# Performance work log

Measured on AMD Instinct MI355X. Metric: run time of the kernel, lower is better.

The kernel has to match this reference:

```python
import jax, jax.numpy as jnp
import numpy as np


def setup_inputs() -> dict:
    key = jax.random.key(0)
    k1, k2, k3, k4 = jax.random.split(key, 4)
    N, E, F_IN, F_OUT = 50000, 800000, 128, 128
    x = jax.random.normal(k1, (N, F_IN), dtype=jnp.float32)
    src = jax.random.randint(k2, (E,), 0, N, dtype=jnp.int32)
    dst = jax.random.randint(k3, (E,), 0, N, dtype=jnp.int32)
    # Linear(2*in, out, bias=False) weight, torch layout (out, 2*in)
    W = jax.random.normal(k4, (F_OUT, 2 * F_IN), dtype=jnp.float32) * (1.0 / np.sqrt(2 * F_IN))
    return {"x": x, "src": src, "dst": dst, "num_nodes": N, "W": W}


def reference(x, src, dst, num_nodes, W):
    # Mean aggregation over sparse adjacency (edge list src -> dst):
    # aggregated[v] = mean_{u in N(v)} x[u]
    msgs = x[src]                                            # [E, F] gather
    summed = jax.ops.segment_sum(msgs, dst, num_segments=num_nodes)  # [N, F]
    deg = jax.ops.segment_sum(jnp.ones_like(dst, dtype=x.dtype), dst,
                              num_segments=num_nodes)        # [N]
    agg = summed / jnp.maximum(deg, 1.0)[:, None]            # mean, safe for isolated nodes
    h = jnp.concatenate([x, agg], axis=1)                    # [N, 2F]
    out = h @ W.T                                            # [N, F_out]
    return jax.nn.relu(out)
```

## Files before the change

### kernel.cpp

```cpp
#include <hip/hip_runtime.h>
#include <hip/hip_bf16.h>

typedef __attribute__((ext_vector_type(8))) short short8;
typedef __attribute__((ext_vector_type(4))) float f32x4;
typedef __attribute__((ext_vector_type(2))) float f32x2;

#define BKS      6
#define BKN      64
#define ITERA    16
#define NBMAX    1024
#define CAPB_MAX 3072

__device__ __forceinline__ unsigned short f2bf(float f) {
    unsigned u = __builtin_bit_cast(unsigned, f);
    u += 0x7fffu + ((u >> 16) & 1u);
    return (unsigned short)(u >> 16);
}
__device__ __forceinline__ float bf2f(unsigned short b) {
    return __builtin_bit_cast(float, ((unsigned)b) << 16);
}

__global__ __launch_bounds__(256) void prepbin_kernel(
    const float* __restrict__ x, unsigned short* __restrict__ xb,
    unsigned char* __restrict__ xq,
    const float* __restrict__ W, unsigned short* __restrict__ Wp,
    const int* __restrict__ src, const int* __restrict__ dst,
    unsigned* gcur, unsigned* __restrict__ gbuf,
    int E, int nb, int capb, int nx8)
{
    __shared__ unsigned cnt[NBMAX];
    __shared__ unsigned gbase[NBMAX];
    int tid = threadIdx.x;
    int gid = blockIdx.x * 256 + tid;
    int gstr = gridDim.x * 256;

    for (int i = gid; i < nx8; i += gstr) {
        const float4* p = (const float4*)(x + (size_t)i * 8);
        float4 lo = p[0], hi = p[1];
        short8 v;
        v[0] = (short)f2bf(lo.x); v[1] = (short)f2bf(lo.y);
        v[2] = (short)f2bf(lo.z); v[3] = (short)f2bf(lo.w);
        v[4] = (short)f2bf(hi.x); v[5] = (short)f2bf(hi.y);
        v[6] = (short)f2bf(hi.z); v[7] = (short)f2bf(hi.w);
        *(short8*)(xb + (size_t)i * 8) = v;

        int p0 = 0, p1 = 0;
        p0 = __builtin_amdgcn_cvt_pk_fp8_f32(lo.x, lo.y, p0, false);
        p0 = __builtin_amdgcn_cvt_pk_fp8_f32(lo.z, lo.w, p0, true);
        p1 = __builtin_amdgcn_cvt_pk_fp8_f32(hi.x, hi.y, p1, false);
        p1 = __builtin_amdgcn_cvt_pk_fp8_f32(hi.z, hi.w, p1, true);
        uint2 q; q.x = (unsigned)p0; q.y = (unsigned)p1;
        *(uint2*)(xq + (size_t)i * 8) = q;
    }
    if (gid < 4096) {
        const float4* p = (const float4*)(W + (size_t)gid * 8);
        float4 lo = p[0], hi = p[1];
        short8 v;
        v[0] = (short)f2bf(lo.x); v[1] = (short)f2bf(lo.y);
        v[2] = (short)f2bf(lo.z); v[3] = (short)f2bf(lo.w);
        v[4] = (short)f2bf(hi.x); v[5] = (short)f2bf(hi.y);
        v[6] = (short)f2bf(hi.z); v[7] = (short)f2bf(hi.w);
        int r    = gid >> 5;
        int c0   = (gid & 31) << 3;
        int ct   = r >> 4;
        int arow = r & 15;
        int ks   = c0 >> 5;
        int kgrp = (c0 >> 3) & 3;
        int l    = arow | (kgrp << 4);
        *(short8*)(Wp + (((size_t)(ct * 8 + ks) * 64 + l) * 8)) = v;
    }

    int EB = (E + 256 * ITERA - 1) / (256 * ITERA);
    if (blockIdx.x < EB) {
        for (int t = tid; t < nb; t += 256) cnt[t] = 0u;
        __syncthreads();

        int e0 = blockIdx.x * (256 * ITERA) + tid;
        unsigned pk[ITERA];
        unsigned short bk[ITERA], pp[ITERA];
#pragma unroll
        for (int it = 0; it < ITERA; ++it) {
            int e = e0 + it * 256;
            bk[it] = 0xFFFFu;
            if (e < E) {
                int d = dst[e];
                unsigned b = (unsigned)d >> BKS;
                pk[it] = (unsigned)src[e] | ((unsigned)(d & (BKN - 1)) << 24);
                pp[it] = (unsigned short)atomicAdd(&cnt[b], 1u);
                bk[it] = (unsigned short)b;
            }
        }
        __syncthreads();
        for (int t = tid; t < nb; t += 256)
            gbase[t] = cnt[t] ? atomicAdd(&gcur[t], cnt[t]) : 0u;
        __syncthreads();
#pragma unroll
        for (int it = 0; it < ITERA; ++it) {
            if (bk[it] != 0xFFFFu) {
                unsigned b = bk[it];
                unsigned off = gbase[b] + pp[it];
                if (off < (unsigned)capb) gbuf[(size_t)b * capb + off] = pk[it];
            }
        }
    }
}

__global__ __launch_bounds__(512) void agg_gemm_kernel(
    const unsigned short* __restrict__ xb,
    const unsigned char* __restrict__ xq,
    const unsigned* __restrict__ gbuf,
    const unsigned* __restrict__ gcur,
    const unsigned short* __restrict__ Wp,
    float* __restrict__ out, int N, int capb)
{
    __shared__ unsigned cnt[BKN];
    __shared__ unsigned degs[BKN];
    __shared__ unsigned cur[BKN];
    __shared__ unsigned elist[CAPB_MAX];
    __shared__ unsigned short aggs[BKN][136];

    int tid = threadIdx.x;
    int b   = blockIdx.x;
    unsigned cntB = gcur[b];
    if (cntB > (unsigned)capb) cntB = (unsigned)capb;
    const unsigned* bb = gbuf + (size_t)b * capb;

    if (tid < BKN) cnt[tid] = 0u;
    __syncthreads();
    for (unsigned i = tid; i < cntB; i += 512)
        atomicAdd(&cnt[bb[i] >> 24], 1u);
    __syncthreads();
    if (tid < BKN) degs[tid] = cnt[tid];
    __syncthreads();
#pragma unroll
    for (int off = 1; off < BKN; off <<= 1) {
        unsigned t = (tid < BKN && tid >= off) ? cnt[tid - off] : 0u;
        __syncthreads();
        if (tid < BKN) cnt[tid] += t;
        __syncthreads();
    }
    if (tid < BKN) cur[tid] = cnt[tid] - degs[tid];
    __syncthreads();
    for (unsigned i = tid; i < cntB; i += 512) {
        unsigned pk = bb[i];
        unsigned p  = atomicAdd(&cur[pk >> 24], 1u);
        elist[p] = pk & 0x00FFFFFFu;
    }
    __syncthreads();

    int wv = tid >> 6, l = tid & 63;
    int q4 = l >> 4, ql = l & 15;
    int base = b << BKS;

#pragma unroll
    for (int pass = 0; pass < BKN / 32; ++pass) {
        int r0 = pass * 32 + wv * 4 + q4;
        unsigned endi  = cnt[r0];
        unsigned dg    = degs[r0];
        unsigned start = endi - dg;
        float acc[8] = {0.f, 0.f, 0.f, 0.f, 0.f, 0.f, 0.f, 0.f};

        for (unsigned eb = start; eb < endi; eb += 4) {
            unsigned last = endi - 1;
            unsigned e1 = eb + 1, e2 = eb + 2, e3 = eb + 3;
            float w0 = 1.0f;
            float w1 = (e1 < endi) ? 1.0f : 0.0f;
            float w2 = (e2 < endi) ? 1.0f : 0.0f;
            float w3 = (e3 < endi) ? 1.0f : 0.0f;
            unsigned i1 = (e1 < endi) ? e1 : last;
            unsigned i2 = (e2 < endi) ? e2 : last;
            unsigned i3 = (e3 < endi) ? e3 : last;
            unsigned s0 = elist[eb], s1 = elist[i1];
            unsigned s2 = elist[i2], s3 = elist[i3];
            uint2 u0 = *(const uint2*)(xq + (size_t)s0 * 128 + ql * 8);
            uint2 u1 = *(const uint2*)(xq + (size_t)s1 * 128 + ql * 8);
            uint2 u2 = *(const uint2*)(xq + (size_t)s2 * 128 + ql * 8);
            uint2 u3 = *(const uint2*)(xq + (size_t)s3 * 128 + ql * 8);
#define ACC8(u, w)                                                            \
            {                                                                 \
                f32x2 a0 = __builtin_amdgcn_cvt_pk_f32_fp8((int)(u).x, false);\
                f32x2 a1 = __builtin_amdgcn_cvt_pk_f32_fp8((int)(u).x, true); \
                f32x2 a2 = __builtin_amdgcn_cvt_pk_f32_fp8((int)(u).y, false);\
                f32x2 a3 = __builtin_amdgcn_cvt_pk_f32_fp8((int)(u).y, true); \
                acc[0] = fmaf(w, a0.x, acc[0]); acc[1] = fmaf(w, a0.y, acc[1]);\
                acc[2] = fmaf(w, a1.x, acc[2]); acc[3] = fmaf(w, a1.y, acc[3]);\
                acc[4] = fmaf(w, a2.x, acc[4]); acc[5] = fmaf(w, a2.y, acc[5]);\
                acc[6] = fmaf(w, a3.x, acc[6]); acc[7] = fmaf(w, a3.y, acc[7]);\
            }
            ACC8(u0, w0); ACC8(u1, w1); ACC8(u2, w2); ACC8(u3, w3);
#undef ACC8
        }

        float inv = dg ? 1.0f / (float)dg : 1.0f;
        short8 st;
#pragma unroll
        for (int j = 0; j < 8; ++j) st[j] = (short)f2bf(acc[j] * inv);
        *(short8*)&aggs[r0][ql * 8] = st;
    }
    __syncthreads();

    int w    = tid >> 6;
    int rt   = w >> 1;
    int cth  = w & 1;
    int arow = l & 15;
    int kgrp = l >> 4;
    int row  = base + rt * 16 + arow;
    bool rok = row < N;

    short8 afrag[8];
#pragma unroll
    for (int ks = 0; ks < 4; ++ks) {
        short8 a = {};
        if (rok) a = *(const short8*)(xb + (size_t)row * 128 + ks * 32 + kgrp * 8);
        afrag[ks] = a;
    }
#pragma unroll
    for (int ks = 0; ks < 4; ++ks)
        afrag[4 + ks] = *(const short8*)&aggs[rt * 16 + arow][ks * 32 + kgrp * 8];

    f32x4 acc[4];
#pragma unroll
    for (int c = 0; c < 4; ++c) acc[c] = (f32x4){0.f, 0.f, 0.f, 0.f};

#pragma unroll
    for (int ks = 0; ks < 8; ++ks) {
        short8 a = afrag[ks];
#pragma unroll
        for (int c = 0; c < 4; ++c) {
            int ct = cth * 4 + c;
            const short8* bp =
                (const short8*)(Wp + (((size_t)(ct * 8 + ks) * 64 + l) * 8));
            acc[c] = __builtin_amdgcn_mfma_f32_16x16x32_bf16(a, *bp, acc[c], 0, 0, 0);
        }
    }

#pragma unroll
    for (int c = 0; c < 4; ++c) {
#pragma unroll
        for (int r = 0; r < 4; ++r) {
            int orow = base + rt * 16 + kgrp * 4 + r;
            if (orow < N) {
                out[(size_t)orow * 128 + (cth * 4 + c) * 16 + arow] =
                    fmaxf(acc[c][r], 0.0f);
            }
        }
    }
}

extern "C" void kernel_launch(void* const* d_in, const int* in_sizes, int n_in,
                              void* d_out, int out_size, void* d_ws, size_t ws_size,
                              hipStream_t stream) {
    const float* x  = (const float*)d_in[0];
    const int* src  = (const int*)d_in[1];
    const int* dst  = (const int*)d_in[2];
    const float* W  = (const float*)d_in[4];

    int N = in_sizes[0] / 128;
    int E = in_sizes[1];
    float* out = (float*)d_out;

    int nb = (N + BKN - 1) >> BKS;
    int capb = 2 * (E / (nb > 0 ? nb : 1)) + 1024;
    capb = (capb + 63) & ~63;
    if (capb > CAPB_MAX) capb = CAPB_MAX;

    char* ws = (char*)d_ws;
    size_t o = 0;
    auto carve = [&](size_t bytes) {
        char* p = ws + o;
        o += (bytes + 255) & ~(size_t)255;
        return p;
    };
    unsigned* gcur     = (unsigned*)carve((size_t)nb * 4);
    unsigned* gbuf     = (unsigned*)carve((size_t)nb * capb * 4);
    unsigned short* Wp = (unsigned short*)carve(128 * 256 * 2);
    unsigned short* xb = (unsigned short*)carve((size_t)N * 128 * 2);
    unsigned char* xq  = (unsigned char*)carve((size_t)N * 128);
    (void)ws_size;

    int nx8 = N * 16;
    int gb  = (nx8 + 255) / 256;
    int eb  = (E + 256 * ITERA - 1) / (256 * ITERA);
    if (gb < eb) gb = eb;
    if (gb < 16) gb = 16;

    hipMemsetAsync(gcur, 0, (size_t)nb * 4, stream);
    prepbin_kernel<<<gb, 256, 0, stream>>>(x, xb, xq, W, Wp, src, dst, gcur, gbuf,
                                           E, nb, capb, nx8);
    agg_gemm_kernel<<<nb, 512, 0, stream>>>(xb, xq, gbuf, gcur, Wp, out, N, capb);
}
```

Measured before the change: 66.68 us.

## Sort edges per block in shared memory before coalesced bucket scatter

The binning blocks now do a local counting sort. They take a histogram, run a block-wide exclusive scan and stage the edges in shared memory in bucket order, then write to the global bucket buffer with consecutive threads hitting consecutive slots. This replaces the earlier scattered per-thread writes. The conversion work (x to bf16/fp8, W packing) moves to separate blocks after the binning blocks instead of a grid-stride loop shared by all blocks. The change adds about 30KB of shared memory and extra barriers per binning block, which may lower occupancy.

Result: no change. 67.45 us (+1.2%).

```diff
diff --git a/kernel.cpp b/kernel.cpp
--- a/kernel.cpp
+++ b/kernel.cpp
@@ -7,7 +7,7 @@
 
 #define BKS      6
 #define BKN      64
-#define ITERA    16
+#define EPB      4096
 #define NBMAX    1024
 #define CAPB_MAX 3072
 
@@ -28,80 +28,112 @@
     unsigned* gcur, unsigned* __restrict__ gbuf,
     int E, int nb, int capb, int nx8)
 {
-    __shared__ unsigned cnt[NBMAX];
-    __shared__ unsigned gbase[NBMAX];
     int tid = threadIdx.x;
-    int gid = blockIdx.x * 256 + tid;
-    int gstr = gridDim.x * 256;
-
-    for (int i = gid; i < nx8; i += gstr) {
-        const float4* p = (const float4*)(x + (size_t)i * 8);
-        float4 lo = p[0], hi = p[1];
-        short8 v;
-        v[0] = (short)f2bf(lo.x); v[1] = (short)f2bf(lo.y);
-        v[2] = (short)f2bf(lo.z); v[3] = (short)f2bf(lo.w);
-        v[4] = (short)f2bf(hi.x); v[5] = (short)f2bf(hi.y);
-        v[6] = (short)f2bf(hi.z); v[7] = (short)f2bf(hi.w);
-        *(short8*)(xb + (size_t)i * 8) = v;
-
-        int p0 = 0, p1 = 0;
-        p0 = __builtin_amdgcn_cvt_pk_fp8_f32(lo.x, lo.y, p0, false);
-        p0 = __builtin_amdgcn_cvt_pk_fp8_f32(lo.z, lo.w, p0, true);
-        p1 = __builtin_amdgcn_cvt_pk_fp8_f32(hi.x, hi.y, p1, false);
-        p1 = __builtin_amdgcn_cvt_pk_fp8_f32(hi.z, hi.w, p1, true);
-        uint2 q; q.x = (unsigned)p0; q.y = (unsigned)p1;
-        *(uint2*)(xq + (size_t)i * 8) = q;
-    }
-    if (gid < 4096) {
-        const float4* p = (const float4*)(W + (size_t)gid * 8);
-        float4 lo = p[0], hi = p[1];
-        short8 v;
-        v[0] = (short)f2bf(lo.x); v[1] = (short)f2bf(lo.y);
-        v[2] = (short)f2bf(lo.z); v[3] = (short)f2bf(lo.w);
-        v[4] = (short)f2bf(hi.x); v[5] = (short)f2bf(hi.y);
-        v[6] = (short)f2bf(hi.z); v[7] = (short)f2bf(hi.w);
-        int r    = gid >> 5;
-        int c0   = (gid & 31) << 3;
-        int ct   = r >> 4;
-        int arow = r & 15;
-        int ks   = c0 >> 5;
-        int kgrp = (c0 >> 3) & 3;
-        int l    = arow | (kgrp << 4);
-        *(short8*)(Wp + (((size_t)(ct * 8 + ks) * 64 + l) * 8)) = v;
-    }
-
-    int EB = (E + 256 * ITERA - 1) / (256 * ITERA);
-    if (blockIdx.x < EB) {
-        for (int t = tid; t < nb; t += 256) cnt[t] = 0u;
+    int EB  = (E + EPB - 1) / EPB;
+
+    if ((int)blockIdx.x >= EB) {
+        int gid = (blockIdx.x - EB) * 256 + tid;
+        if (gid < nx8) {
+            const float4* p = (const float4*)(x + (size_t)gid * 8);
+            float4 lo = p[0], hi = p[1];
+            short8 v;
+            v[0] = (short)f2bf(lo.x); v[1] = (short)f2bf(lo.y);
+            v[2] = (short)f2bf(lo.z); v[3] = (short)f2bf(lo.w);
+            v[4] = (short)f2bf(hi.x); v[5] = (short)f2bf(hi.y);
+            v[6] = (short)f2bf(hi.z); v[7] = (short)f2bf(hi.w);
+            *(short8*)(xb + (size_t)gid * 8) = v;
+
+            int p0 = 0, p1 = 0;
+            p0 = __builtin_amdgcn_cvt_pk_fp8_f32(lo.x, lo.y, p0, false);
+            p0 = __builtin_amdgcn_cvt_pk_fp8_f32(lo.z, lo.w, p0, true);
+            p1 = __builtin_amdgcn_cvt_pk_fp8_f32(hi.x, hi.y, p1, false);
+            p1 = __builtin_amdgcn_cvt_pk_fp8_f32(hi.z, hi.w, p1, true);
+            uint2 q; q.x = (unsigned)p0; q.y = (unsigned)p1;
+            *(uint2*)(xq + (size_t)gid * 8) = q;
+        }
+        if (gid < 4096) {
+            const float4* p = (const float4*)(W + (size_t)gid * 8);
+            float4 lo = p[0], hi = p[1];
+            short8 v;
+            v[0] = (short)f2bf(lo.x); v[1] = (short)f2bf(lo.y);
+            v[2] = (short)f2bf(lo.z); v[3] = (short)f2bf(lo.w);
+            v[4] = (short)f2bf(hi.x); v[5] = (short)f2bf(hi.y);
+            v[6] = (short)f2bf(hi.z); v[7] = (short)f2bf(hi.w);
+            int r    = gid >> 5;
+            int c0   = (gid & 31) << 3;
+            int ct   = r >> 4;
+            int arow = r & 15;
+            int ks   = c0 >> 5;
+            int kgrp = (c0 >> 3) & 3;
+            int l    = arow | (kgrp << 4);
+            *(short8*)(Wp + (((size_t)(ct * 8 + ks) * 64 + l) * 8)) = v;
+        }
+        return;
+    }
+
+    __shared__ unsigned hist[NBMAX];
+    __shared__ unsigned excl[NBMAX];
+    __shared__ unsigned sbase[NBMAX];
+    __shared__ unsigned part[256];
+    __shared__ unsigned sedge[EPB];
+    __shared__ unsigned short sbkt[EPB];
+
+    for (int t = tid; t < nb; t += 256) hist[t] = 0u;
+    __syncthreads();
+
+    int e0 = blockIdx.x * EPB + tid;
+    unsigned pk[EPB / 256];
+    unsigned short bk[EPB / 256], pp[EPB / 256];
+#pragma unroll
+    for (int it = 0; it < EPB / 256; ++it) {
+        int e = e0 + it * 256;
+        bk[it] = 0xFFFFu;
+        if (e < E) {
+            int d = dst[e];
+            unsigned b = (unsigned)d >> BKS;
+            pk[it] = (unsigned)src[e] | ((unsigned)(d & (BKN - 1)) << 24);
+            pp[it] = (unsigned short)atomicAdd(&hist[b], 1u);
+            bk[it] = (unsigned short)b;
+        }
+    }
+    __syncthreads();
+
+    int ch = (nb + 255) >> 8;
+    int b0 = tid * ch;
+    int b1 = b0 + ch; if (b1 > nb) b1 = nb;
+    unsigned s = 0;
+    for (int i = b0; i < b1; ++i) s += hist[i];
+    part[tid] = s;
+    __syncthreads();
+#pragma unroll
+    for (int off = 1; off < 256; off <<= 1) {
+        unsigned t = (tid >= off) ? part[tid - off] : 0u;
         __syncthreads();
-
-        int e0 = blockIdx.x * (256 * ITERA) + tid;
-        unsigned pk[ITERA];
-        unsigned short bk[ITERA], pp[ITERA];
-#pragma unroll
-        for (int it = 0; it < ITERA; ++it) {
-            int e = e0 + it * 256;
-            bk[it] = 0xFFFFu;
-            if (e < E) {
-                int d = dst[e];
-                unsigned b = (unsigned)d >> BKS;
-                pk[it] = (unsigned)src[e] | ((unsigned)(d & (BKN - 1)) << 24);
-                pp[it] = (unsigned short)atomicAdd(&cnt[b], 1u);
-                bk[it] = (unsigned short)b;
-            }
-        }
+        part[tid] += t;
         __syncthreads();
-        for (int t = tid; t < nb; t += 256)
-            gbase[t] = cnt[t] ? atomicAdd(&gcur[t], cnt[t]) : 0u;
-        __syncthreads();
-#pragma unroll
-        for (int it = 0; it < ITERA; ++it) {
-            if (bk[it] != 0xFFFFu) {
-                unsigned b = bk[it];
-                unsigned off = gbase[b] + pp[it];
-                if (off < (unsigned)capb) gbuf[(size_t)b * capb + off] = pk[it];
-            }
-        }
+    }
+    unsigned run = part[tid] - s;
+    for (int i = b0; i < b1; ++i) { excl[i] = run; run += hist[i]; }
+    __syncthreads();
+
+#pragma unroll
+    for (int it = 0; it < EPB / 256; ++it) {
+        if (bk[it] != 0xFFFFu) {
+            unsigned b = bk[it];
+            unsigned pos = excl[b] + pp[it];
+            sedge[pos] = pk[it];
+            sbkt[pos]  = (unsigned short)b;
+        }
+    }
+    for (int t = tid; t < nb; t += 256)
+        sbase[t] = hist[t] ? atomicAdd(&gcur[t], hist[t]) : 0u;
+    __syncthreads();
+
+    unsigned total = excl[nb - 1] + hist[nb - 1];
+    for (unsigned i = tid; i < total; i += 256) {
+        unsigned b   = sbkt[i];
+        unsigned off = sbase[b] + (i - excl[b]);
+        if (off < (unsigned)capb) gbuf[(size_t)b * capb + off] = sedge[i];
     }
 }
 
@@ -279,13 +311,12 @@
     (void)ws_size;
 
     int nx8 = N * 16;
-    int gb  = (nx8 + 255) / 256;
-    int eb  = (E + 256 * ITERA - 1) / (256 * ITERA);
-    if (gb < eb) gb = eb;
-    if (gb < 16) gb = 16;
+    int EB  = (E + EPB - 1) / EPB;
+    int CB  = (nx8 + 255) / 256;
+    if (CB < 16) CB = 16;
 
     hipMemsetAsync(gcur, 0, (size_t)nb * 4, stream);
-    prepbin_kernel<<<gb, 256, 0, stream>>>(x, xb, xq, W, Wp, src, dst, gcur, gbuf,
-                                           E, nb, capb, nx8);
+    prepbin_kernel<<<EB + CB, 256, 0, stream>>>(x, xb, xq, W, Wp, src, dst,
+                                                gcur, gbuf, E, nb, capb, nx8);
     agg_gemm_kernel<<<nb, 512, 0, stream>>>(xb, xq, gbuf, gcur, Wp, out, N, capb);
 }
```

## Fuse prep, binning and aggregation-GEMM into one cooperative persistent kernel

Applied to the files above, without the earlier changes.

Replaces the memset plus two-kernel pipeline with a single cooperative kernel. It converts x and W, then after a grid sync bins edges into per-bucket lists, and after another grid sync processes buckets through an atomic ticket work queue that does the aggregation and the MFMA GEMM. The self-feature bf16 copy of x is dropped; x is converted from fp32 inside the GEMM stage instead. This removes launch gaps and the xb write/read, at the cost of two grid-wide barriers, a grid sized at about nb/2 blocks that must be co-resident, and large shared-memory use per block. The old two-kernel path is kept as a fallback if the cooperative launch fails.

New measurement: 194.3 us. 2.91x slower.

```diff
diff --git a/kernel.cpp b/kernel.cpp
--- a/kernel.cpp
+++ b/kernel.cpp
@@ -1,5 +1,8 @@
 #include <hip/hip_runtime.h>
 #include <hip/hip_bf16.h>
+#include <hip/hip_cooperative_groups.h>
+
+namespace cg = cooperative_groups;
 
 typedef __attribute__((ext_vector_type(8))) short short8;
 typedef __attribute__((ext_vector_type(4))) float f32x4;
@@ -7,43 +10,42 @@
 
 #define BKS      6
 #define BKN      64
-#define ITERA    16
 #define NBMAX    1024
 #define CAPB_MAX 3072
+#define EPC      2048
+#define EPB      4096
 
 __device__ __forceinline__ unsigned short f2bf(float f) {
     unsigned u = __builtin_bit_cast(unsigned, f);
     u += 0x7fffu + ((u >> 16) & 1u);
     return (unsigned short)(u >> 16);
 }
-__device__ __forceinline__ float bf2f(unsigned short b) {
-    return __builtin_bit_cast(float, ((unsigned)b) << 16);
-}
-
-__global__ __launch_bounds__(256) void prepbin_kernel(
-    const float* __restrict__ x, unsigned short* __restrict__ xb,
-    unsigned char* __restrict__ xq,
+
+__global__ __launch_bounds__(512, 4) void coop_kernel(
+    const float* __restrict__ x, unsigned char* __restrict__ xq,
     const float* __restrict__ W, unsigned short* __restrict__ Wp,
     const int* __restrict__ src, const int* __restrict__ dst,
-    unsigned* gcur, unsigned* __restrict__ gbuf,
-    int E, int nb, int capb, int nx8)
+    unsigned* gcur, unsigned* __restrict__ gbuf, unsigned* ticket,
+    float* __restrict__ out, int N, int E, int nb, int capb, int nx8)
 {
-    __shared__ unsigned cnt[NBMAX];
-    __shared__ unsigned gbase[NBMAX];
-    int tid = threadIdx.x;
-    int gid = blockIdx.x * 256 + tid;
-    int gstr = gridDim.x * 256;
+    cg::grid_group grid = cg::this_grid();
+
+    __shared__ unsigned h_cnt[NBMAX];
+    __shared__ unsigned h_base[NBMAX];
+    __shared__ unsigned cntA[BKN];
+    __shared__ unsigned degs[BKN];
+    __shared__ unsigned curA[BKN];
+    __shared__ unsigned elist[CAPB_MAX];
+    __shared__ unsigned short aggs[BKN][136];
+    __shared__ unsigned tkt;
+
+    int tid  = threadIdx.x;
+    int gid  = blockIdx.x * 512 + tid;
+    int gstr = gridDim.x * 512;
 
     for (int i = gid; i < nx8; i += gstr) {
         const float4* p = (const float4*)(x + (size_t)i * 8);
         float4 lo = p[0], hi = p[1];
-        short8 v;
-        v[0] = (short)f2bf(lo.x); v[1] = (short)f2bf(lo.y);
-        v[2] = (short)f2bf(lo.z); v[3] = (short)f2bf(lo.w);
-        v[4] = (short)f2bf(hi.x); v[5] = (short)f2bf(hi.y);
-        v[6] = (short)f2bf(hi.z); v[7] = (short)f2bf(hi.w);
-        *(short8*)(xb + (size_t)i * 8) = v;
-
         int p0 = 0, p1 = 0;
         p0 = __builtin_amdgcn_cvt_pk_fp8_f32(lo.x, lo.y, p0, false);
         p0 = __builtin_amdgcn_cvt_pk_fp8_f32(lo.z, lo.w, p0, true);
@@ -69,17 +71,247 @@
         int l    = arow | (kgrp << 4);
         *(short8*)(Wp + (((size_t)(ct * 8 + ks) * 64 + l) * 8)) = v;
     }
-
-    int EB = (E + 256 * ITERA - 1) / (256 * ITERA);
-    if (blockIdx.x < EB) {
+    for (int i = gid; i < nb; i += gstr) gcur[i] = 0u;
+    if (gid == 0) *ticket = 0u;
+
+    grid.sync();
+
+    int nchunks = (E + EPC - 1) / EPC;
+    for (int ch = blockIdx.x; ch < nchunks; ch += gridDim.x) {
+        for (int t = tid; t < nb; t += 512) h_cnt[t] = 0u;
+        __syncthreads();
+        int e0 = ch * EPC + tid;
+        unsigned pk[EPC / 512];
+        unsigned short bk[EPC / 512], pp[EPC / 512];
+#pragma unroll
+        for (int it = 0; it < EPC / 512; ++it) {
+            int e = e0 + it * 512;
+            bk[it] = 0xFFFFu;
+            if (e < E) {
+                int d = dst[e];
+                unsigned b = (unsigned)d >> BKS;
+                pk[it] = (unsigned)src[e] | ((unsigned)(d & (BKN - 1)) << 24);
+                pp[it] = (unsigned short)atomicAdd(&h_cnt[b], 1u);
+                bk[it] = (unsigned short)b;
+            }
+        }
+        __syncthreads();
+        for (int t = tid; t < nb; t += 512)
+            h_base[t] = h_cnt[t] ? atomicAdd(&gcur[t], h_cnt[t]) : 0u;
+        __syncthreads();
+#pragma unroll
+        for (int it = 0; it < EPC / 512; ++it) {
+            if (bk[it] != 0xFFFFu) {
+                unsigned b = bk[it];
+                unsigned off = h_base[b] + pp[it];
+                if (off < (unsigned)capb) gbuf[(size_t)b * capb + off] = pk[it];
+            }
+        }
+        __syncthreads();
+    }
+
+    grid.sync();
+
+    int wv = tid >> 6, l = tid & 63;
+    int q4 = l >> 4, ql = l & 15;
+
+    while (true) {
+        __syncthreads();
+        if (tid == 0) tkt = atomicAdd(ticket, 1u);
+        __syncthreads();
+        unsigned b = tkt;
+        if (b >= (unsigned)nb) break;
+
+        unsigned cntB = gcur[b];
+        if (cntB > (unsigned)capb) cntB = (unsigned)capb;
+        const unsigned* bb = gbuf + (size_t)b * capb;
+        int base = (int)b << BKS;
+
+        if (tid < BKN) cntA[tid] = 0u;
+        __syncthreads();
+        for (unsigned i = tid; i < cntB; i += 512)
+            atomicAdd(&cntA[bb[i] >> 24], 1u);
+        __syncthreads();
+        if (tid < BKN) degs[tid] = cntA[tid];
+        __syncthreads();
+#pragma unroll
+        for (int off = 1; off < BKN; off <<= 1) {
+            unsigned t = (tid < BKN && tid >= off) ? cntA[tid - off] : 0u;
+            __syncthreads();
+            if (tid < BKN) cntA[tid] += t;
+            __syncthreads();
+        }
+        if (tid < BKN) curA[tid] = cntA[tid] - degs[tid];
+        __syncthreads();
+        for (unsigned i = tid; i < cntB; i += 512) {
+            unsigned pk = bb[i];
+            unsigned p  = atomicAdd(&curA[pk >> 24], 1u);
+            elist[p] = pk & 0x00FFFFFFu;
+        }
+        __syncthreads();
+
+#pragma unroll
+        for (int pass = 0; pass < BKN / 32; ++pass) {
+            int r0 = pass * 32 + wv * 4 + q4;
+            unsigned endi  = cntA[r0];
+            unsigned dg    = degs[r0];
+            unsigned start = endi - dg;
+            float acc[8] = {0.f, 0.f, 0.f, 0.f, 0.f, 0.f, 0.f, 0.f};
+
+            for (unsigned eb = start; eb < endi; eb += 4) {
+                unsigned last = endi - 1;
+                unsigned e1 = eb + 1, e2 = eb + 2, e3 = eb + 3;
+                float w0 = 1.0f;
+                float w1 = (e1 < endi) ? 1.0f : 0.0f;
+                float w2 = (e2 < endi) ? 1.0f : 0.0f;
+                float w3 = (e3 < endi) ? 1.0f : 0.0f;
+                unsigned i1 = (e1 < endi) ? e1 : last;
+                unsigned i2 = (e2 < endi) ? e2 : last;
+                unsigned i3 = (e3 < endi) ? e3 : last;
+                unsigned s0 = elist[eb], s1 = elist[i1];
+                unsigned s2 = elist[i2], s3 = elist[i3];
+                uint2 u0 = *(const uint2*)(xq + (size_t)s0 * 128 + ql * 8);
+                uint2 u1 = *(const uint2*)(xq + (size_t)s1 * 128 + ql * 8);
+                uint2 u2 = *(const uint2*)(xq + (size_t)s2 * 128 + ql * 8);
+                uint2 u3 = *(const uint2*)(xq + (size_t)s3 * 128 + ql * 8);
+#define ACC8(u, w)                                                            \
+                {                                                             \
+                    f32x2 a0 = __builtin_amdgcn_cvt_pk_f32_fp8((int)(u).x, false);\
+                    f32x2 a1 = __builtin_amdgcn_cvt_pk_f32_fp8((int)(u).x, true); \
+                    f32x2 a2 = __builtin_amdgcn_cvt_pk_f32_fp8((int)(u).y, false);\
+                    f32x2 a3 = __builtin_amdgcn_cvt_pk_f32_fp8((int)(u).y, true); \
+                    acc[0] = fmaf(w, a0.x, acc[0]); acc[1] = fmaf(w, a0.y, acc[1]);\
+                    acc[2] = fmaf(w, a1.x, acc[2]); acc[3] = fmaf(w, a1.y, acc[3]);\
+                    acc[4] = fmaf(w, a2.x, acc[4]); acc[5] = fmaf(w, a2.y, acc[5]);\
+                    acc[6] = fmaf(w, a3.x, acc[6]); acc[7] = fmaf(w, a3.y, acc[7]);\
+                }
+                ACC8(u0, w0); ACC8(u1, w1); ACC8(u2, w2); ACC8(u3, w3);
+#undef ACC8
+            }
+
+            float inv = dg ? 1.0f / (float)dg : 1.0f;
+            short8 st;
+#pragma unroll
+            for (int j = 0; j < 8; ++j) st[j] = (short)f2bf(acc[j] * inv);
+            *(short8*)&aggs[r0][ql * 8] = st;
+        }
+        __syncthreads();
+
+        int w    = tid >> 6;
+        int rt   = w >> 1;
+        int cth  = w & 1;
+        int arow = l & 15;
+        int kgrp = l >> 4;
+        int row  = base + rt * 16 + arow;
+        bool rok = row < N;
+
+        short8 afrag[8];
+#pragma unroll
+        for (int ks = 0; ks < 4; ++ks) {
+            short8 a = {};
+            if (rok) {
+                const float4* p = (const float4*)(x + (size_t)row * 128 + ks * 32 + kgrp * 8);
+                float4 lo = p[0], hi = p[1];
+                a[0] = (short)f2bf(lo.x); a[1] = (short)f2bf(lo.y);
+                a[2] = (short)f2bf(lo.z); a[3] = (short)f2bf(lo.w);
+                a[4] = (short)f2bf(hi.x); a[5] = (short)f2bf(hi.y);
+                a[6] = (short)f2bf(hi.z); a[7] = (short)f2bf(hi.w);
+            }
+            afrag[ks] = a;
+        }
+#pragma unroll
+        for (int ks = 0; ks < 4; ++ks)
+            afrag[4 + ks] = *(const short8*)&aggs[rt * 16 + arow][ks * 32 + kgrp * 8];
+
+        f32x4 acc2[4];
+#pragma unroll
+        for (int c = 0; c < 4; ++c) acc2[c] = (f32x4){0.f, 0.f, 0.f, 0.f};
+
+#pragma unroll
+        for (int ks = 0; ks < 8; ++ks) {
+            short8 a = afrag[ks];
+#pragma unroll
+            for (int c = 0; c < 4; ++c) {
+                int ct = cth * 4 + c;
+                const short8* bp =
+                    (const short8*)(Wp + (((size_t)(ct * 8 + ks) * 64 + l) * 8));
+                acc2[c] = __builtin_amdgcn_mfma_f32_16x16x32_bf16(a, *bp, acc2[c], 0, 0, 0);
+            }
+        }
+
+#pragma unroll
+        for (int c = 0; c < 4; ++c) {
+#pragma unroll
+            for (int r = 0; r < 4; ++r) {
+                int orow = base + rt * 16 + kgrp * 4 + r;
+                if (orow < N) {
+                    out[(size_t)orow * 128 + (cth * 4 + c) * 16 + arow] =
+                        fmaxf(acc2[c][r], 0.0f);
+                }
+            }
+        }
+    }
+}
+
+__global__ __launch_bounds__(256) void prepbin_kernel(
+    const float* __restrict__ x, unsigned short* __restrict__ xb,
+    unsigned char* __restrict__ xq,
+    const float* __restrict__ W, unsigned short* __restrict__ Wp,
+    const int* __restrict__ src, const int* __restrict__ dst,
+    unsigned* gcur, unsigned* __restrict__ gbuf,
+    int E, int nb, int capb, int nx8)
+{
+    __shared__ unsigned cnt[NBMAX];
+    __shared__ unsigned gbase[NBMAX];
+    int tid = threadIdx.x;
+    int gid = blockIdx.x * 256 + tid;
+    int gstr = gridDim.x * 256;
+
+    for (int i = gid; i < nx8; i += gstr) {
+        const float4* p = (const float4*)(x + (size_t)i * 8);
+        float4 lo = p[0], hi = p[1];
+        short8 v;
+        v[0] = (short)f2bf(lo.x); v[1] = (short)f2bf(lo.y);
+        v[2] = (short)f2bf(lo.z); v[3] = (short)f2bf(lo.w);
+        v[4] = (short)f2bf(hi.x); v[5] = (short)f2bf(hi.y);
+        v[6] = (short)f2bf(hi.z); v[7] = (short)f2bf(hi.w);
+        *(short8*)(xb + (size_t)i * 8) = v;
+
+        int p0 = 0, p1 = 0;
+        p0 = __builtin_amdgcn_cvt_pk_fp8_f32(lo.x, lo.y, p0, false);
+        p0 = __builtin_amdgcn_cvt_pk_fp8_f32(lo.z, lo.w, p0, true);
+        p1 = __builtin_amdgcn_cvt_pk_fp8_f32(hi.x, hi.y, p1, false);
+        p1 = __builtin_amdgcn_cvt_pk_fp8_f32(hi.z, hi.w, p1, true);
+        uint2 q; q.x = (unsigned)p0; q.y = (unsigned)p1;
+        *(uint2*)(xq + (size_t)i * 8) = q;
+    }
+    if (gid < 4096) {
+        const float4* p = (const float4*)(W + (size_t)gid * 8);
+        float4 lo = p[0], hi = p[1];
+        short8 v;
+        v[0] = (short)f2bf(lo.x); v[1] = (short)f2bf(lo.y);
+        v[2] = (short)f2bf(lo.z); v[3] = (short)f2bf(lo.w);
+        v[4] = (short)f2bf(hi.x); v[5] = (short)f2bf(hi.y);
+        v[6] = (short)f2bf(hi.z); v[7] = (short)f2bf(hi.w);
+        int r    = gid >> 5;
+        int c0   = (gid & 31) << 3;
+        int ct   = r >> 4;
+        int arow = r & 15;
+        int ks   = c0 >> 5;
+        int kgrp = (c0 >> 3) & 3;
+        int l    = arow | (kgrp << 4);
+        *(short8*)(Wp + (((size_t)(ct * 8 + ks) * 64 + l) * 8)) = v;
+    }
+
+    int EB = (E + EPB - 1) / EPB;
+    if ((int)blockIdx.x < EB) {
         for (int t = tid; t < nb; t += 256) cnt[t] = 0u;
         __syncthreads();
-
-        int e0 = blockIdx.x * (256 * ITERA) + tid;
-        unsigned pk[ITERA];
-        unsigned short bk[ITERA], pp[ITERA];
-#pragma unroll
-        for (int it = 0; it < ITERA; ++it) {
+        int e0 = blockIdx.x * EPB + tid;
+        unsigned pk[EPB / 256];
+        unsigned short bk[EPB / 256], pp[EPB / 256];
+#pragma unroll
+        for (int it = 0; it < EPB / 256; ++it) {
             int e = e0 + it * 256;
             bk[it] = 0xFFFFu;
             if (e < E) {
@@ -95,7 +327,7 @@
             gbase[t] = cnt[t] ? atomicAdd(&gcur[t], cnt[t]) : 0u;
         __syncthreads();
 #pragma unroll
-        for (int it = 0; it < ITERA; ++it) {
+        for (int it = 0; it < EPB / 256; ++it) {
             if (bk[it] != 0xFFFFu) {
                 unsigned b = bk[it];
                 unsigned off = gbase[b] + pp[it];
@@ -272,6 +504,7 @@
         return p;
     };
     unsigned* gcur     = (unsigned*)carve((size_t)nb * 4);
+    unsigned* ticket   = (unsigned*)carve(256);
     unsigned* gbuf     = (unsigned*)carve((size_t)nb * capb * 4);
     unsigned short* Wp = (unsigned short*)carve(128 * 256 * 2);
     unsigned short* xb = (unsigned short*)carve((size_t)N * 128 * 2);
@@ -279,13 +512,30 @@
     (void)ws_size;
 
     int nx8 = N * 16;
-    int gb  = (nx8 + 255) / 256;
-    int eb  = (E + 256 * ITERA - 1) / (256 * ITERA);
-    if (gb < eb) gb = eb;
-    if (gb < 16) gb = 16;
-
-    hipMemsetAsync(gcur, 0, (size_t)nb * 4, stream);
-    prepbin_kernel<<<gb, 256, 0, stream>>>(x, xb, xq, W, Wp, src, dst, gcur, gbuf,
-                                           E, nb, capb, nx8);
-    agg_gemm_kernel<<<nb, 512, 0, stream>>>(xb, xq, gbuf, gcur, Wp, out, N, capb);
+    int nblocks = (nb + 1) / 2;
+    if (nblocks < 1) nblocks = 1;
+
+    unsigned char* xq_ = xq;
+    unsigned short* Wp_ = Wp;
+    unsigned* gcur_ = gcur;
+    unsigned* gbuf_ = gbuf;
+    unsigned* ticket_ = ticket;
+    void* args[] = {(void*)&x, (void*)&xq_, (void*)&W, (void*)&Wp_,
+                    (void*)&src, (void*)&dst, (void*)&gcur_, (void*)&gbuf_,
+                    (void*)&ticket_, (void*)&out, (void*)&N, (void*)&E,
+                    (void*)&nb, (void*)&capb, (void*)&nx8};
+
+    hipError_t err = hipLaunchCooperativeKernel((const void*)coop_kernel,
+                                                dim3(nblocks), dim3(512),
+                                                args, 0, stream);
+    if (err != hipSuccess) {
+        int EB = (E + EPB - 1) / EPB;
+        int CB = (nx8 + 255) / 256;
+        int gb = (EB > CB ? EB : CB);
+        if (gb < 16) gb = 16;
+        hipMemsetAsync(gcur, 0, (size_t)nb * 4, stream);
+        prepbin_kernel<<<gb, 256, 0, stream>>>(x, xb, xq, W, Wp, src, dst,
+                                               gcur, gbuf, E, nb, capb, nx8);
+        agg_gemm_kernel<<<nb, 512, 0, stream>>>(xb, xq, gbuf, gcur, Wp, out, N, capb);
+    }
 }
```
